# Optimization experiments

Measured on AMD Instinct MI355X. Metric: run time of the kernel, lower is better.

The kernel has to match this reference:

```python
import jax, jax.numpy as jnp
import numpy as np


def setup_inputs() -> dict:
    key = jax.random.key(0)
    k1, k2 = jax.random.split(key)
    N, C, H, W = 64, 256, 64, 64
    T, V, M = 64, 25, 2
    rgb_feature = jax.random.normal(k1, (N, C, H, W), dtype=jnp.float32)
    skeleton_seq = jax.random.uniform(k2, (N, 3, T, V, M), dtype=jnp.float32)
    return {"rgb_feature": rgb_feature, "skeleton_seq": skeleton_seq}


def reference(rgb_feature, skeleton_seq):
    N, C, H, W = rgb_feature.shape
    T = skeleton_seq.shape[2]
    first_frame = skeleton_seq[:, :, 0, :, :]        # (N, 3, V, M)
    mid_frame = skeleton_seq[:, :, T // 2, :, :]     # (N, 3, V, M)
    # joint displacement magnitude, averaged over persons M
    distances = jnp.linalg.norm(mid_frame - first_frame, axis=1)  # (N, V, M)
    distances = distances.mean(axis=2)                            # (N, V)
    max_dist_idx = jnp.argmax(distances, axis=1)                  # (N,)
    # gather (x, y) of selected joint, person 0
    joint_pos = jnp.take_along_axis(
        mid_frame[:, :2, :, 0], max_dist_idx[:, None, None], axis=2
    )[:, :, 0]                                                    # (N, 2)
    # torch does int(v.item()) -> truncation toward zero; grad is cut by .item()
    joint_pos = jax.lax.stop_gradient(joint_pos)
    x_pos = jnp.trunc(joint_pos[:, 0] * W)                        # (N,)
    y_pos = jnp.trunc(joint_pos[:, 1] * H)                        # (N,)
    y_grid = jnp.arange(H, dtype=jnp.float32)[:, None]            # (H, 1)
    x_grid = jnp.arange(W, dtype=jnp.float32)[None, :]            # (1, W)
    sigma = min(H, W) * 0.15
    # per-sample gaussian bump centered at the fastest-moving joint
    gaussian = jnp.exp(
        -((x_grid[None] - x_pos[:, None, None]) ** 2
          + (y_grid[None] - y_pos[:, None, None]) ** 2)
        / (2.0 * sigma ** 2)
    )                                                             # (N, H, W)
    attention_mask = jax.nn.sigmoid(gaussian)[:, None, :, :]      # (N, 1, H, W)
    return rgb_feature * attention_mask
```

## Files before the change

kernel.cpp:

```cpp
#include <hip/hip_runtime.h>
#include <hip/hip_bf16.h>

#define NN 64
#define CC 256
#define HH 64
#define WW 64
#define TT 64
#define VV 25
#define MM 2

__global__ void skel_center_kernel(const float* __restrict__ skel,
                                   float* __restrict__ xy) {
    int n = threadIdx.x;
    if (n >= NN) return;
    const int sC = TT * VV * MM;
    const int sT = VV * MM;
    const float* base = skel + n * 3 * sC;
    const float* mid = base + (TT / 2) * sT;

    int best_v = 0;
    float best_d = -1.0f;
#pragma unroll 5
    for (int v = 0; v < VV; ++v) {
        float sum = 0.0f;
#pragma unroll
        for (int m = 0; m < MM; ++m) {
            float s2 = 0.0f;
#pragma unroll
            for (int c = 0; c < 3; ++c) {
                float f0 = base[c * sC + v * MM + m];
                float fm = mid[c * sC + v * MM + m];
                float d = fm - f0;
                s2 += d * d;
            }
            sum += sqrtf(s2);
        }
        float dist = sum * 0.5f;
        if (dist > best_d) { best_d = dist; best_v = v; }
    }
    float jx = mid[0 * sC + best_v * MM + 0];
    float jy = mid[1 * sC + best_v * MM + 0];
    xy[n]      = truncf(jx * (float)WW);
    xy[NN + n] = truncf(jy * (float)HH);
}

__global__ void apply_mask_kernel(const float* __restrict__ rgb,
                                  const float* __restrict__ xy,
                                  float* __restrict__ out) {
    const float inv_2s2 = 1.0f / (2.0f * 9.6f * 9.6f);
    const int total4 = NN * CC * HH * WW / 4;
    int stride = gridDim.x * blockDim.x;
    for (int i = blockIdx.x * blockDim.x + threadIdx.x; i < total4; i += stride) {
        int n    = i >> 18;
        int rem  = i & ((1 << 18) - 1);
        int hw4  = rem & 1023;
        int h    = hw4 >> 4;
        int w0   = (hw4 & 15) << 2;

        float xp = xy[n];
        float yp = xy[NN + n];
        float dy = (float)h - yp;
        float dy2 = dy * dy;

        float4 r = reinterpret_cast<const float4*>(rgb)[i];
        float4 o;
#pragma unroll
        for (int j = 0; j < 4; ++j) {
            float dx = (float)(w0 + j) - xp;
            float g = __expf(-(dx * dx + dy2) * inv_2s2);
            float m = 1.0f / (1.0f + __expf(-g));
            (&o.x)[j] = (&r.x)[j] * m;
        }
        reinterpret_cast<float4*>(out)[i] = o;
    }
}

extern "C" void kernel_launch(void* const* d_in, const int* in_sizes, int n_in,
                              void* d_out, int out_size, void* d_ws, size_t ws_size,
                              hipStream_t stream) {
    const float* rgb  = (const float*)d_in[0];
    const float* skel = (const float*)d_in[1];
    float* out = (float*)d_out;
    float* xy  = (float*)d_ws;

    skel_center_kernel<<<1, 64, 0, stream>>>(skel, xy);

    int block = 256;
    int grid = 4096;
    apply_mask_kernel<<<grid, block, 0, stream>>>(rgb, xy, out);
}
```

Measured before the change: 447.6 us.

## Precompute per-sample mask once, apply with nontemporal vector loads/stores

The first kernel now runs one block per sample. It uses a wave shuffle argmax to find the joint and writes the full HxW sigmoid-gaussian mask into workspace, so the mask is no longer recomputed for every channel. The apply kernel becomes a pure multiply of rgb by the cached mask, using nontemporal loads and stores on the streaming data. This removes two expf calls per element from the bandwidth-bound pass. In exchange it adds a 1 MB mask read that should stay in cache, and it needs the workspace to be large enough.

```diff
diff --git a/kernel.cpp b/kernel.cpp
--- a/kernel.cpp
+++ b/kernel.cpp
@@ -9,69 +9,88 @@
 #define VV 25
 #define MM 2
 
-__global__ void skel_center_kernel(const float* __restrict__ skel,
-                                   float* __restrict__ xy) {
-    int n = threadIdx.x;
-    if (n >= NN) return;
+typedef float f4 __attribute__((ext_vector_type(4)));
+
+__global__ __launch_bounds__(256) void build_mask_kernel(
+    const float* __restrict__ skel, float* __restrict__ mask) {
+    const int n  = blockIdx.x;
     const int sC = TT * VV * MM;
     const int sT = VV * MM;
     const float* base = skel + n * 3 * sC;
-    const float* mid = base + (TT / 2) * sT;
+    const float* mid  = base + (TT / 2) * sT;
 
-    int best_v = 0;
-    float best_d = -1.0f;
-#pragma unroll 5
-    for (int v = 0; v < VV; ++v) {
-        float sum = 0.0f;
+    __shared__ float s_xy[2];
+    const int tid = threadIdx.x;
+
+    if (tid < 64) {
+        float d = -1.0f;
+        int   v = tid;
+        if (tid < VV) {
+            float sum = 0.0f;
 #pragma unroll
-        for (int m = 0; m < MM; ++m) {
-            float s2 = 0.0f;
+            for (int m = 0; m < MM; ++m) {
+                float s2 = 0.0f;
 #pragma unroll
-            for (int c = 0; c < 3; ++c) {
-                float f0 = base[c * sC + v * MM + m];
-                float fm = mid[c * sC + v * MM + m];
-                float d = fm - f0;
-                s2 += d * d;
+                for (int c = 0; c < 3; ++c) {
+                    float f0 = base[c * sC + tid * MM + m];
+                    float fm = mid [c * sC + tid * MM + m];
+                    float df = fm - f0;
+                    s2 += df * df;
+                }
+                sum += sqrtf(s2);
             }
-            sum += sqrtf(s2);
+            d = sum * 0.5f;
         }
-        float dist = sum * 0.5f;
-        if (dist > best_d) { best_d = dist; best_v = v; }
+#pragma unroll
+        for (int off = 16; off >= 1; off >>= 1) {
+            float od = __shfl_xor(d, off, 32);
+            int   ov = __shfl_xor(v, off, 32);
+            if (od > d || (od == d && ov < v)) { d = od; v = ov; }
+        }
+        if (tid == 0) {
+            float jx = mid[0 * sC + v * MM + 0];
+            float jy = mid[1 * sC + v * MM + 0];
+            s_xy[0] = truncf(jx * (float)WW);
+            s_xy[1] = truncf(jy * (float)HH);
+        }
     }
-    float jx = mid[0 * sC + best_v * MM + 0];
-    float jy = mid[1 * sC + best_v * MM + 0];
-    xy[n]      = truncf(jx * (float)WW);
-    xy[NN + n] = truncf(jy * (float)HH);
-}
+    __syncthreads();
 
-__global__ void apply_mask_kernel(const float* __restrict__ rgb,
-                                  const float* __restrict__ xy,
-                                  float* __restrict__ out) {
+    const float xp = s_xy[0];
+    const float yp = s_xy[1];
     const float inv_2s2 = 1.0f / (2.0f * 9.6f * 9.6f);
-    const int total4 = NN * CC * HH * WW / 4;
-    int stride = gridDim.x * blockDim.x;
-    for (int i = blockIdx.x * blockDim.x + threadIdx.x; i < total4; i += stride) {
-        int n    = i >> 18;
-        int rem  = i & ((1 << 18) - 1);
-        int hw4  = rem & 1023;
-        int h    = hw4 >> 4;
-        int w0   = (hw4 & 15) << 2;
 
-        float xp = xy[n];
-        float yp = xy[NN + n];
-        float dy = (float)h - yp;
+    for (int idx = tid; idx < HH * WW / 4; idx += 256) {
+        int h  = idx >> 4;
+        int w0 = (idx & 15) << 2;
+        float dy  = (float)h - yp;
         float dy2 = dy * dy;
-
-        float4 r = reinterpret_cast<const float4*>(rgb)[i];
-        float4 o;
+        f4 o;
 #pragma unroll
         for (int j = 0; j < 4; ++j) {
             float dx = (float)(w0 + j) - xp;
             float g = __expf(-(dx * dx + dy2) * inv_2s2);
-            float m = 1.0f / (1.0f + __expf(-g));
-            (&o.x)[j] = (&r.x)[j] * m;
+            o[j] = 1.0f / (1.0f + __expf(-g));
         }
-        reinterpret_cast<float4*>(out)[i] = o;
+        reinterpret_cast<f4*>(mask)[(n << 10) | idx] = o;
+    }
+}
+
+__global__ __launch_bounds__(256) void apply_mask_kernel(
+    const float* __restrict__ rgb, const float* __restrict__ mask,
+    float* __restrict__ out) {
+    const int total4 = NN * CC * HH * WW / 4;
+    const int stride = gridDim.x * blockDim.x;
+    const f4* rgb4 = reinterpret_cast<const f4*>(rgb);
+    const f4* m4   = reinterpret_cast<const f4*>(mask);
+    f4* out4 = reinterpret_cast<f4*>(out);
+    for (int i = blockIdx.x * blockDim.x + threadIdx.x; i < total4; i += stride) {
+        int n   = i >> 18;
+        int hw4 = i & 1023;
+        f4 r = __builtin_nontemporal_load(&rgb4[i]);
+        f4 m = m4[(n << 10) | hw4];
+        f4 o = r * m;
+        __builtin_nontemporal_store(o, &out4[i]);
     }
 }
 
@@ -80,12 +99,9 @@
                               hipStream_t stream) {
     const float* rgb  = (const float*)d_in[0];
     const float* skel = (const float*)d_in[1];
-    float* out = (float*)d_out;
-    float* xy  = (float*)d_ws;
+    float* out  = (float*)d_out;
+    float* mask = (float*)d_ws;
 
-    skel_center_kernel<<<1, 64, 0, stream>>>(skel, xy);
-
-    int block = 256;
-    int grid = 4096;
-    apply_mask_kernel<<<grid, block, 0, stream>>>(rgb, xy, out);
+    build_mask_kernel<<<NN, 256, 0, stream>>>(skel, mask);
+    apply_mask_kernel<<<4096, 256, 0, stream>>>(rgb, mask, out);
 }
```

Result: faster. 430.7 us (-3.8%).
